# Kernel tuning notes

Measured on AMD Instinct MI355X. Metric: run time of the kernel, lower is better.

The kernel has to match this reference:

```python
import jax, jax.numpy as jnp
import numpy as np

D_IN, H1, H2, B, K = 128, 128, 64, 262144, 4

def _mk(key, shape):
    return jax.random.normal(key, shape, dtype=jnp.float32) * 0.05

def setup_inputs() -> dict:
    key = jax.random.key(0)
    ks = jax.random.split(key, 40)
    inp = {
        'x': jax.random.normal(ks[0], (B, 96), dtype=jnp.float32),
        'u': jax.random.normal(ks[1], (B, 32), dtype=jnp.float32),
        'mix_factor': jax.random.uniform(ks[2], (1,), dtype=jnp.float32),
        'teacher_P': jax.random.uniform(ks[3], (K,), dtype=jnp.float32),
    }
    # main critic params (torch Linear: W [out,in], b [out])
    dims = [(H1, D_IN), (H1, H1), (H2, H1), (1, H2)] * 2  # l1..l4, l5..l8
    for i, (o, ii) in enumerate(dims):
        inp[f'W{i+1}'] = _mk(ks[4 + 2 * i], (o, ii))
        inp[f'b{i+1}'] = _mk(ks[5 + 2 * i], (o,))
    # stacked teacher params (K teachers), only l1,l2,l3,l5,l6,l7 are used
    tdims = {'1': (H1, D_IN), '2': (H1, H1), '3': (H2, H1), '5': (H1, D_IN), '6': (H1, H1), '7': (H2, H1)}
    j = 20
    for name, (o, ii) in tdims.items():
        inp[f'tW{name}'] = _mk(ks[j], (K, o, ii)); j += 1
        inp[f'tb{name}'] = _mk(ks[j], (K, o)); j += 1
    return inp

def reference(x, u, mix_factor, teacher_P, W1, b1, W2, b2, W3, b3, W4, b4, W5, b5, W6, b6, W7, b7, W8, b8, tW1, tb1, tW2, tb2, tW3, tb3, tW5, tb5, tW6, tb6, tW7, tb7):
    m = mix_factor  # [1], broadcasts
    P = teacher_P   # [K]
    xu = jnp.concatenate([x, u], axis=1)  # [B, 128]

    lin = lambda h, W, b: h @ W.T + b
    # teacher linear on shared input [B,I] -> [K,B,O]
    tlin0 = lambda h, W, b: jnp.einsum('bi,koi->kbo', h, W) + b[:, None, :]
    # teacher linear on per-teacher streams [K,B,I] -> [K,B,O]
    tlin = lambda h, W, b: jnp.einsum('kbi,koi->kbo', h, W) + b[:, None, :]
    mixsum = lambda ht: jnp.einsum('kbo,k->bo', ht, P)

    def head(W_a, b_a, W_b, b_b, W_c, b_c, W_d, b_d, tWa, tba, tWb, tbb, tWc, tbc):
        ht = tlin0(xu, tWa, tba)                                   # [K,B,128]
        h = jax.nn.relu(lin(xu, W_a, b_a) * (1 - m) + mixsum(ht) * m)
        ht = jax.nn.relu(ht)
        ht2 = tlin(ht, tWb, tbb)
        h = jax.nn.relu(lin(h, W_b, b_b) * (1 - m) + mixsum(ht2) * m)
        ht2 = jax.nn.relu(ht2)
        ht3 = tlin(ht2, tWc, tbc)
        h = jax.nn.relu(lin(h, W_c, b_c) * (1 - m) + mixsum(ht3) * m)
        return lin(h, W_d, b_d)                                    # [B,1]

    x1 = head(W1, b1, W2, b2, W3, b3, W4, b4, tW1, tb1, tW2, tb2, tW3, tb3)
    x2 = head(W5, b5, W6, b6, W7, b7, W8, b8, tW5, tb5, tW6, tb6, tW7, tb7)
    return (x1, x2)
```

## Files before the change

kernel.cpp:

```cpp
#include <hip/hip_runtime.h>
#include <hip/hip_bf16.h>
#include <stdint.h>

#define B_TOTAL 262144
#define TB 64
#define RECORD 2560
#define LDS_BYTES 163840
#define HEAD_W 204800

typedef short v8s __attribute__((ext_vector_type(8)));
typedef float v4f __attribute__((ext_vector_type(4)));

union Frag { uint4 q; uint32_t d[4]; v8s v; };

__device__ __forceinline__ uint32_t pack2(float a, float b) {
    union { __hip_bfloat162 h; uint32_t u; } p;
    p.h = __float22bfloat162_rn(make_float2(a, b));
    return p.u;
}


struct KParams {
    const float* x; const float* u; const float* mix; const float* P;
    const float* mb[6];
    const float* tb[6];
    const float* Wout[2];
    const float* bout[2];
    const unsigned short* wbf;
    float* out;
};

struct PrepParams { const float* src[12]; unsigned short* dst; };

__global__ __launch_bounds__(256) void prep_kernel(PrepParams pp) {
    const int ends[12] = {16384,81920,98304,163840,172032,204800,
                          221184,286720,303104,368640,376832,409600};
    int gi = (blockIdx.x * 256 + threadIdx.x) * 4;
    if (gi >= 409600) return;
    int s = 0;
    #pragma unroll
    for (int i = 0; i < 12; ++i) { if (gi >= ends[i]) s = i + 1; }
    int base = (s == 0) ? 0 : ends[s - 1];
    const float4 f = *(const float4*)(pp.src[s] + (gi - base));
    *(uint2*)(pp.dst + gi) = make_uint2(pack2(f.x, f.y), pack2(f.z, f.w));
}

__device__ __forceinline__ void stage_xu(char* lds, const float* x, const float* u,
                                         int rowBase, int tid)
{
    for (int G = tid; G < 1024; G += 512) {
        const int row = G >> 4;
        const int gg  = G & 15;
        const int grow = rowBase + row;
        float4 fa, fb;
        if (gg < 12) {
            const float* s2 = x + grow * 96 + gg * 8;
            fa = *(const float4*)s2; fb = *(const float4*)(s2 + 4);
        } else {
            const float* s2 = u + grow * 32 + (gg - 12) * 8;
            fa = *(const float4*)s2; fb = *(const float4*)(s2 + 4);
        }
        *(uint4*)(lds + row * RECORD + ((gg ^ (row & 15)) << 4)) =
            make_uint4(pack2(fa.x, fa.y), pack2(fa.z, fa.w),
                       pack2(fb.x, fb.y), pack2(fb.z, fb.w));
    }
}

struct WPre { Frag w[20]; float4 mB; float4 tB[4]; };

template<int N>
__device__ __forceinline__ WPre preload(const unsigned short* W, int colBase,
        const float* mbias, const float* tbias, int lane)
{
    WPre r;
    const int l15  = lane & 15;
    const int quad = lane >> 4;
    const unsigned short* wRow = W + (colBase + l15) * 128 + quad * 8;
    #pragma unroll
    for (int s = 0; s < 5; ++s)
        #pragma unroll
        for (int ks = 0; ks < 4; ++ks)
            r.w[s * 4 + ks].q = *(const uint4*)(wRow + s * (N * 128) + ks * 32);
    const int obase = colBase + quad * 4;
    r.mB = *(const float4*)(mbias + obase);
    #pragma unroll
    for (int s = 0; s < 4; ++s)
        r.tB[s] = *(const float4*)(tbias + s * N + obase);
    return r;
}

template<bool SHARED_IN, int SM, int ST, int NBT>
__device__ __forceinline__ void mfma_phase(const char* lds, uint32_t btOff,
        const WPre& wp, v4f (&acc)[5][NBT], int lane)
{
    const int l15  = lane & 15;
    const int quad = lane >> 4;
    const uint32_t rb = (uint32_t)l15 * RECORD + ((uint32_t)l15 << 4) + btOff;
    uint32_t rA[4];
    #pragma unroll
    for (int ks = 0; ks < 4; ++ks)
        rA[ks] = rb ^ (uint32_t)(((ks << 2) | quad) << 4);

    #pragma unroll
    for (int bt = 0; bt < NBT; ++bt) {
        acc[0][bt] = (v4f){wp.mB.x, wp.mB.y, wp.mB.z, wp.mB.w};
        #pragma unroll
        for (int s = 0; s < 4; ++s)
            acc[s + 1][bt] = (v4f){wp.tB[s].x, wp.tB[s].y, wp.tB[s].z, wp.tB[s].w};
    }

    #pragma unroll
    for (int ks = 0; ks < 4; ++ks) {
        Frag xS[NBT];
        if constexpr (SHARED_IN) {
            #pragma unroll
            for (int bt = 0; bt < NBT; ++bt)
                xS[bt].q = *(const uint4*)(lds + rA[ks]
                            + (uint32_t)(bt * 40960 + SM * 256));
        }
        #pragma unroll
        for (int s = 0; s < 5; ++s) {
            constexpr int dummy = 0; (void)dummy;
            Frag xF[NBT];
            if constexpr (!SHARED_IN) {
                const int slot = (s == 0) ? SM : (ST + s - 1);
                #pragma unroll
                for (int bt = 0; bt < NBT; ++bt)
                    xF[bt].q = *(const uint4*)(lds + rA[ks]
                                + (uint32_t)(bt * 40960 + slot * 256));
            }
            #pragma unroll
            for (int bt = 0; bt < NBT; ++bt)
                acc[s][bt] = __builtin_amdgcn_mfma_f32_16x16x32_bf16(
                    wp.w[s * 4 + ks].v, (SHARED_IN ? xS[bt].v : xF[bt].v),
                    acc[s][bt], 0, 0, 0);
        }
    }
}

template<int WM, int WT>
__device__ __forceinline__ void write_streams(char* lds, v4f (&acc)[5][4],
        float c0, const float* cP, int lane, int colBase)
{
    const int l15  = lane & 15;
    const int quad = lane >> 4;
    const uint32_t rb = (uint32_t)l15 * RECORD + ((uint32_t)l15 << 4);
    const int ocg = (colBase >> 3) + (quad >> 1);
    const uint32_t w0 = (rb ^ ((uint32_t)ocg << 4)) + (uint32_t)((quad & 1) << 3);
    #pragma unroll
    for (int bt = 0; bt < 4; ++bt) {
        char* ab = lds + (w0 + (uint32_t)(bt * 40960));
        float vr[4];
        vr[0] = c0 * acc[0][bt][0];
        vr[1] = c0 * acc[0][bt][1];
        vr[2] = c0 * acc[0][bt][2];
        vr[3] = c0 * acc[0][bt][3];
        uint2 tw[4];
        #pragma unroll
        for (int s = 0; s < 4; ++s) {
            const float t0 = acc[s + 1][bt][0];
            const float t1 = acc[s + 1][bt][1];
            const float t2 = acc[s + 1][bt][2];
            const float t3 = acc[s + 1][bt][3];
            vr[0] = fmaf(cP[s], t0, vr[0]);
            vr[1] = fmaf(cP[s], t1, vr[1]);
            vr[2] = fmaf(cP[s], t2, vr[2]);
            vr[3] = fmaf(cP[s], t3, vr[3]);
            tw[s] = make_uint2(pack2(fmaxf(t0, 0.f), fmaxf(t1, 0.f)),
                               pack2(fmaxf(t2, 0.f), fmaxf(t3, 0.f)));
        }
        *(uint2*)(ab + WM * 256) =
            make_uint2(pack2(fmaxf(vr[0], 0.f), fmaxf(vr[1], 0.f)),
                       pack2(fmaxf(vr[2], 0.f), fmaxf(vr[3], 0.f)));
        #pragma unroll
        for (int s = 0; s < 4; ++s)
            *(uint2*)(ab + (WT + s) * 256) = tw[s];
    }
}

__device__ __forceinline__ void psum_write(const v4f (&accF)[5][2], float c0,
        const float* cP, const float* Wout, float* pgrid, int lane,
        int cb64, int btB64)
{
    const int obase = cb64 + ((lane >> 4) << 2);
    const float4 wo = *(const float4*)(Wout + obase);
    #pragma unroll
    for (int j = 0; j < 2; ++j) {
        float vr[4];
        vr[0] = c0 * accF[0][j][0];
        vr[1] = c0 * accF[0][j][1];
        vr[2] = c0 * accF[0][j][2];
        vr[3] = c0 * accF[0][j][3];
        #pragma unroll
        for (int s = 0; s < 4; ++s) {
            vr[0] = fmaf(cP[s], accF[s + 1][j][0], vr[0]);
            vr[1] = fmaf(cP[s], accF[s + 1][j][1], vr[1]);
            vr[2] = fmaf(cP[s], accF[s + 1][j][2], vr[2]);
            vr[3] = fmaf(cP[s], accF[s + 1][j][3], vr[3]);
        }
        float pp = fmaxf(vr[0], 0.f) * wo.x + fmaxf(vr[1], 0.f) * wo.y
                 + fmaxf(vr[2], 0.f) * wo.z + fmaxf(vr[3], 0.f) * wo.w;
        pp += __shfl_xor(pp, 16);
        pp += __shfl_xor(pp, 32);
        if (lane < 16)
            pgrid[(cb64 >> 4) * 64 + (btB64 + j) * 16 + lane] = pp;
    }
}

extern "C" __global__ __launch_bounds__(512, 2)
void critic_kernel(KParams p)
{
    extern __shared__ char lds[];
    const int tid  = threadIdx.x;
    const int lane = tid & 63;
    const int wave = tid >> 6;
    const int rowBase = blockIdx.x * TB;

    const int cb128 = wave << 4;
    const int cb64  = (wave >> 1) << 4;
    const int btB64 = (wave & 1) << 1;
    const uint32_t btOff64 = (uint32_t)btB64 * 40960u;

    const float m  = p.mix[0];
    const float c0 = 1.f - m;
    float cP[4];
    #pragma unroll
    for (int k = 0; k < 4; ++k) cP[k] = m * p.P[k];

    const unsigned short* wb0 = p.wbf;
    const unsigned short* wb1 = p.wbf + HEAD_W;

    stage_xu(lds, p.x, p.u, rowBase, tid);
    WPre wA = preload<128>(wb0, cb128, p.mb[0], p.tb[0], lane);
    __syncthreads();

    v4f accB[5][4];
    {
        WPre wB = preload<128>(wb1, cb128, p.mb[3], p.tb[3], lane);
        v4f accA[5][4];
        mfma_phase<true, 0, 0, 4>(lds, 0, wA, accA, lane);
        write_streams<1, 2>(lds, accA, c0, cP, lane, cb128);
        mfma_phase<true, 0, 0, 4>(lds, 0, wB, accB, lane);
    }
    __syncthreads();

    v4f accC[5][4];
    {
        WPre wC = preload<128>(wb0 + 81920, cb128, p.mb[1], p.tb[1], lane);
        write_streams<0, 6>(lds, accB, c0, cP, lane, cb128);
        mfma_phase<false, 1, 2, 4>(lds, 0, wC, accC, lane);
    }
    __syncthreads();

    v4f accD[5][4];
    {
        WPre wD = preload<128>(wb1 + 81920, cb128, p.mb[4], p.tb[4], lane);
        write_streams<1, 2>(lds, accC, c0, cP, lane, cb128);
        mfma_phase<false, 0, 6, 4>(lds, 0, wD, accD, lane);
    }
    __syncthreads();

    v4f accE[5][2];
    {
        WPre wE = preload<64>(wb0 + 163840, cb64, p.mb[2], p.tb[2], lane);
        write_streams<0, 6>(lds, accD, c0, cP, lane, cb128);
        mfma_phase<false, 1, 2, 2>(lds, btOff64, wE, accE, lane);
    }
    __syncthreads();

    v4f accF[5][2];
    {
        WPre wF = preload<64>(wb1 + 163840, cb64, p.mb[5], p.tb[5], lane);
        psum_write(accE, c0, cP, p.Wout[0], (float*)(lds + 256),
                   lane, cb64, btB64);
        mfma_phase<false, 0, 6, 2>(lds, btOff64, wF, accF, lane);
    }
    __syncthreads();

    if (tid < 64) {
        const float* pg = (const float*)(lds + 256);
        p.out[rowBase + tid] =
            p.bout[0][0] + pg[tid] + pg[64 + tid] + pg[128 + tid] + pg[192 + tid];
    }
    psum_write(accF, c0, cP, p.Wout[1], (float*)(lds + 1536),
               lane, cb64, btB64);
    __syncthreads();

    if (tid < 64) {
        const float* pg = (const float*)(lds + 1536);
        p.out[B_TOTAL + rowBase + tid] =
            p.bout[1][0] + pg[tid] + pg[64 + tid] + pg[128 + tid] + pg[192 + tid];
    }
}

extern "C" void kernel_launch(void* const* d_in, const int* in_sizes, int n_in,
                              void* d_out, int out_size, void* d_ws, size_t ws_size,
                              hipStream_t stream)
{
    (void)in_sizes; (void)n_in; (void)out_size; (void)ws_size;

    PrepParams pp;
    const int sidx[12] = {4, 20, 6, 22, 8, 24, 12, 26, 14, 28, 16, 30};
    for (int i = 0; i < 12; ++i) pp.src[i] = (const float*)d_in[sidx[i]];
    pp.dst = (unsigned short*)d_ws;

    KParams kp;
    kp.x = (const float*)d_in[0];  kp.u = (const float*)d_in[1];
    kp.mix = (const float*)d_in[2]; kp.P = (const float*)d_in[3];
    const int mbi[6] = {5, 7, 9, 13, 15, 17};
    const int tbi[6] = {21, 23, 25, 27, 29, 31};
    for (int i = 0; i < 6; ++i) {
        kp.mb[i] = (const float*)d_in[mbi[i]];
        kp.tb[i] = (const float*)d_in[tbi[i]];
    }
    kp.Wout[0] = (const float*)d_in[10]; kp.Wout[1] = (const float*)d_in[18];
    kp.bout[0] = (const float*)d_in[11]; kp.bout[1] = (const float*)d_in[19];
    kp.wbf = (const unsigned short*)d_ws;
    kp.out = (float*)d_out;

    (void)hipFuncSetAttribute((const void*)critic_kernel,
                              hipFuncAttributeMaxDynamicSharedMemorySize, LDS_BYTES);

    hipLaunchKernelGGL(prep_kernel, dim3(400), dim3(256), 0, stream, pp);
    hipLaunchKernelGGL(critic_kernel, dim3(B_TOTAL / TB), dim3(512), LDS_BYTES, stream, kp);
}
```

Before: 786.5 us.

## Split weight preloads across K-halves and defer bias add to epilogue

Weight fragment preloads for the next layer are split into two K-halves and interleaved with the current layer's MFMA halves, so global loads overlap matrix work across phase boundaries. Bias is no longer used to initialise the accumulators: they start at zero and bias is added in the write_streams/psum_write epilogues, which frees the bias registers during the MFMA loops. This is meant to hide global load latency and lower register pressure, but it keeps two weight sets partially live at once, which can raise VGPR usage under the 512x2 launch bounds.

```diff
diff --git a/kernel.cpp b/kernel.cpp
--- a/kernel.cpp
+++ b/kernel.cpp
@@ -66,67 +66,57 @@
     }
 }
 
-struct WPre { Frag w[20]; float4 mB; float4 tB[4]; };
-
-template<int N>
-__device__ __forceinline__ WPre preload(const unsigned short* W, int colBase,
-        const float* mbias, const float* tbias, int lane)
-{
-    WPre r;
+struct WPre { Frag w[20]; };
+
+template<int N, int KB, int KE>
+__device__ __forceinline__ void preload_ks(WPre& r, const unsigned short* W,
+        int colBase, int lane)
+{
     const int l15  = lane & 15;
     const int quad = lane >> 4;
     const unsigned short* wRow = W + (colBase + l15) * 128 + quad * 8;
     #pragma unroll
     for (int s = 0; s < 5; ++s)
         #pragma unroll
-        for (int ks = 0; ks < 4; ++ks)
+        for (int ks = KB; ks < KE; ++ks)
             r.w[s * 4 + ks].q = *(const uint4*)(wRow + s * (N * 128) + ks * 32);
-    const int obase = colBase + quad * 4;
-    r.mB = *(const float4*)(mbias + obase);
-    #pragma unroll
-    for (int s = 0; s < 4; ++s)
-        r.tB[s] = *(const float4*)(tbias + s * N + obase);
-    return r;
-}
-
-template<bool SHARED_IN, int SM, int ST, int NBT>
-__device__ __forceinline__ void mfma_phase(const char* lds, uint32_t btOff,
+}
+
+template<int NBT>
+__device__ __forceinline__ void zero_acc(v4f (&acc)[5][NBT]) {
+    #pragma unroll
+    for (int s = 0; s < 5; ++s)
+        #pragma unroll
+        for (int bt = 0; bt < NBT; ++bt)
+            acc[s][bt] = (v4f){0.f, 0.f, 0.f, 0.f};
+}
+
+template<bool SHARED_IN, int SM, int ST, int NBT, int KB, int KE>
+__device__ __forceinline__ void mfma_part(const char* lds, uint32_t btOff,
         const WPre& wp, v4f (&acc)[5][NBT], int lane)
 {
     const int l15  = lane & 15;
     const int quad = lane >> 4;
     const uint32_t rb = (uint32_t)l15 * RECORD + ((uint32_t)l15 << 4) + btOff;
-    uint32_t rA[4];
-    #pragma unroll
-    for (int ks = 0; ks < 4; ++ks)
-        rA[ks] = rb ^ (uint32_t)(((ks << 2) | quad) << 4);
-
-    #pragma unroll
-    for (int bt = 0; bt < NBT; ++bt) {
-        acc[0][bt] = (v4f){wp.mB.x, wp.mB.y, wp.mB.z, wp.mB.w};
-        #pragma unroll
-        for (int s = 0; s < 4; ++s)
-            acc[s + 1][bt] = (v4f){wp.tB[s].x, wp.tB[s].y, wp.tB[s].z, wp.tB[s].w};
-    }
-
-    #pragma unroll
-    for (int ks = 0; ks < 4; ++ks) {
+
+    #pragma unroll
+    for (int ks = KB; ks < KE; ++ks) {
+        const uint32_t rA = rb ^ (uint32_t)(((ks << 2) | quad) << 4);
         Frag xS[NBT];
         if constexpr (SHARED_IN) {
             #pragma unroll
             for (int bt = 0; bt < NBT; ++bt)
-                xS[bt].q = *(const uint4*)(lds + rA[ks]
+                xS[bt].q = *(const uint4*)(lds + rA
                             + (uint32_t)(bt * 40960 + SM * 256));
         }
         #pragma unroll
         for (int s = 0; s < 5; ++s) {
-            constexpr int dummy = 0; (void)dummy;
             Frag xF[NBT];
             if constexpr (!SHARED_IN) {
                 const int slot = (s == 0) ? SM : (ST + s - 1);
                 #pragma unroll
                 for (int bt = 0; bt < NBT; ++bt)
-                    xF[bt].q = *(const uint4*)(lds + rA[ks]
+                    xF[bt].q = *(const uint4*)(lds + rA
                                 + (uint32_t)(bt * 40960 + slot * 256));
             }
             #pragma unroll
@@ -138,12 +128,20 @@
     }
 }
 
-template<int WM, int WT>
+template<int WM, int WT, int N>
 __device__ __forceinline__ void write_streams(char* lds, v4f (&acc)[5][4],
-        float c0, const float* cP, int lane, int colBase)
+        float c0, const float* cP, int lane, int colBase,
+        const float* mbias, const float* tbias)
 {
     const int l15  = lane & 15;
     const int quad = lane >> 4;
+    const int obase = colBase + (quad << 2);
+    const float4 mB = *(const float4*)(mbias + obase);
+    float4 tB[4];
+    #pragma unroll
+    for (int s = 0; s < 4; ++s)
+        tB[s] = *(const float4*)(tbias + s * N + obase);
+
     const uint32_t rb = (uint32_t)l15 * RECORD + ((uint32_t)l15 << 4);
     const int ocg = (colBase >> 3) + (quad >> 1);
     const uint32_t w0 = (rb ^ ((uint32_t)ocg << 4)) + (uint32_t)((quad & 1) << 3);
@@ -151,17 +149,17 @@
     for (int bt = 0; bt < 4; ++bt) {
         char* ab = lds + (w0 + (uint32_t)(bt * 40960));
         float vr[4];
-        vr[0] = c0 * acc[0][bt][0];
-        vr[1] = c0 * acc[0][bt][1];
-        vr[2] = c0 * acc[0][bt][2];
-        vr[3] = c0 * acc[0][bt][3];
+        vr[0] = c0 * (acc[0][bt][0] + mB.x);
+        vr[1] = c0 * (acc[0][bt][1] + mB.y);
+        vr[2] = c0 * (acc[0][bt][2] + mB.z);
+        vr[3] = c0 * (acc[0][bt][3] + mB.w);
         uint2 tw[4];
         #pragma unroll
         for (int s = 0; s < 4; ++s) {
-            const float t0 = acc[s + 1][bt][0];
-            const float t1 = acc[s + 1][bt][1];
-            const float t2 = acc[s + 1][bt][2];
-            const float t3 = acc[s + 1][bt][3];
+            const float t0 = acc[s + 1][bt][0] + tB[s].x;
+            const float t1 = acc[s + 1][bt][1] + tB[s].y;
+            const float t2 = acc[s + 1][bt][2] + tB[s].z;
+            const float t3 = acc[s + 1][bt][3] + tB[s].w;
             vr[0] = fmaf(cP[s], t0, vr[0]);
             vr[1] = fmaf(cP[s], t1, vr[1]);
             vr[2] = fmaf(cP[s], t2, vr[2]);
@@ -179,24 +177,29 @@
 }
 
 __device__ __forceinline__ void psum_write(const v4f (&accF)[5][2], float c0,
-        const float* cP, const float* Wout, float* pgrid, int lane,
-        int cb64, int btB64)
+        const float* cP, const float* Wout, const float* mbias,
+        const float* tbias, float* pgrid, int lane, int cb64, int btB64)
 {
     const int obase = cb64 + ((lane >> 4) << 2);
+    const float4 mB = *(const float4*)(mbias + obase);
+    float4 tB[4];
+    #pragma unroll
+    for (int s = 0; s < 4; ++s)
+        tB[s] = *(const float4*)(tbias + s * 64 + obase);
     const float4 wo = *(const float4*)(Wout + obase);
     #pragma unroll
     for (int j = 0; j < 2; ++j) {
         float vr[4];
-        vr[0] = c0 * accF[0][j][0];
-        vr[1] = c0 * accF[0][j][1];
-        vr[2] = c0 * accF[0][j][2];
-        vr[3] = c0 * accF[0][j][3];
+        vr[0] = c0 * (accF[0][j][0] + mB.x);
+        vr[1] = c0 * (accF[0][j][1] + mB.y);
+        vr[2] = c0 * (accF[0][j][2] + mB.z);
+        vr[3] = c0 * (accF[0][j][3] + mB.w);
         #pragma unroll
         for (int s = 0; s < 4; ++s) {
-            vr[0] = fmaf(cP[s], accF[s + 1][j][0], vr[0]);
-            vr[1] = fmaf(cP[s], accF[s + 1][j][1], vr[1]);
-            vr[2] = fmaf(cP[s], accF[s + 1][j][2], vr[2]);
-            vr[3] = fmaf(cP[s], accF[s + 1][j][3], vr[3]);
+            vr[0] = fmaf(cP[s], accF[s + 1][j][0] + tB[s].x, vr[0]);
+            vr[1] = fmaf(cP[s], accF[s + 1][j][1] + tB[s].y, vr[1]);
+            vr[2] = fmaf(cP[s], accF[s + 1][j][2] + tB[s].z, vr[2]);
+            vr[3] = fmaf(cP[s], accF[s + 1][j][3] + tB[s].w, vr[3]);
         }
         float pp = fmaxf(vr[0], 0.f) * wo.x + fmaxf(vr[1], 0.f) * wo.y
                  + fmaxf(vr[2], 0.f) * wo.z + fmaxf(vr[3], 0.f) * wo.w;
@@ -230,50 +233,70 @@
     const unsigned short* wb0 = p.wbf;
     const unsigned short* wb1 = p.wbf + HEAD_W;
 
+    WPre wA, wB, wC, wD, wE, wF;
+
     stage_xu(lds, p.x, p.u, rowBase, tid);
-    WPre wA = preload<128>(wb0, cb128, p.mb[0], p.tb[0], lane);
+    preload_ks<128, 0, 4>(wA, wb0, cb128, lane);
     __syncthreads();
 
     v4f accB[5][4];
     {
-        WPre wB = preload<128>(wb1, cb128, p.mb[3], p.tb[3], lane);
+        preload_ks<128, 0, 2>(wB, wb1, cb128, lane);
         v4f accA[5][4];
-        mfma_phase<true, 0, 0, 4>(lds, 0, wA, accA, lane);
-        write_streams<1, 2>(lds, accA, c0, cP, lane, cb128);
-        mfma_phase<true, 0, 0, 4>(lds, 0, wB, accB, lane);
+        zero_acc(accA);
+        mfma_part<true, 0, 0, 4, 0, 2>(lds, 0, wA, accA, lane);
+        preload_ks<128, 2, 4>(wB, wb1, cb128, lane);
+        mfma_part<true, 0, 0, 4, 2, 4>(lds, 0, wA, accA, lane);
+        write_streams<1, 2, 128>(lds, accA, c0, cP, lane, cb128,
+                                 p.mb[0], p.tb[0]);
+        zero_acc(accB);
+        mfma_part<true, 0, 0, 4, 0, 4>(lds, 0, wB, accB, lane);
     }
     __syncthreads();
 
     v4f accC[5][4];
     {
-        WPre wC = preload<128>(wb0 + 81920, cb128, p.mb[1], p.tb[1], lane);
-        write_streams<0, 6>(lds, accB, c0, cP, lane, cb128);
-        mfma_phase<false, 1, 2, 4>(lds, 0, wC, accC, lane);
+        preload_ks<128, 0, 4>(wC, wb0 + 81920, cb128, lane);
+        preload_ks<128, 0, 2>(wD, wb1 + 81920, cb128, lane);
+        write_streams<0, 6, 128>(lds, accB, c0, cP, lane, cb128,
+                                 p.mb[3], p.tb[3]);
+        zero_acc(accC);
+        mfma_part<false, 1, 2, 4, 0, 2>(lds, 0, wC, accC, lane);
+        preload_ks<128, 2, 4>(wD, wb1 + 81920, cb128, lane);
+        mfma_part<false, 1, 2, 4, 2, 4>(lds, 0, wC, accC, lane);
     }
     __syncthreads();
 
     v4f accD[5][4];
     {
-        WPre wD = preload<128>(wb1 + 81920, cb128, p.mb[4], p.tb[4], lane);
-        write_streams<1, 2>(lds, accC, c0, cP, lane, cb128);
-        mfma_phase<false, 0, 6, 4>(lds, 0, wD, accD, lane);
+        preload_ks<64, 0, 2>(wE, wb0 + 163840, cb64, lane);
+        write_streams<1, 2, 128>(lds, accC, c0, cP, lane, cb128,
+                                 p.mb[1], p.tb[1]);
+        zero_acc(accD);
+        mfma_part<false, 0, 6, 4, 0, 2>(lds, 0, wD, accD, lane);
+        preload_ks<64, 2, 4>(wE, wb0 + 163840, cb64, lane);
+        mfma_part<false, 0, 6, 4, 2, 4>(lds, 0, wD, accD, lane);
     }
     __syncthreads();
 
     v4f accE[5][2];
     {
-        WPre wE = preload<64>(wb0 + 163840, cb64, p.mb[2], p.tb[2], lane);
-        write_streams<0, 6>(lds, accD, c0, cP, lane, cb128);
-        mfma_phase<false, 1, 2, 2>(lds, btOff64, wE, accE, lane);
+        preload_ks<64, 0, 2>(wF, wb1 + 163840, cb64, lane);
+        write_streams<0, 6, 128>(lds, accD, c0, cP, lane, cb128,
+                                 p.mb[4], p.tb[4]);
+        zero_acc(accE);
+        mfma_part<false, 1, 2, 2, 0, 2>(lds, btOff64, wE, accE, lane);
+        preload_ks<64, 2, 4>(wF, wb1 + 163840, cb64, lane);
+        mfma_part<false, 1, 2, 2, 2, 4>(lds, btOff64, wE, accE, lane);
     }
     __syncthreads();
 
     v4f accF[5][2];
     {
-        WPre wF = preload<64>(wb1 + 163840, cb64, p.mb[5], p.tb[5], lane);
-        psum_write(accE, c0, cP, p.Wout[0], (float*)(lds + 256),
-                   lane, cb64, btB64);
-        mfma_phase<false, 0, 6, 2>(lds, btOff64, wF, accF, lane);
+        zero_acc(accF);
+        psum_write(accE, c0, cP, p.Wout[0], p.mb[2], p.tb[2],
+                   (float*)(lds + 256), lane, cb64, btB64);
+        mfma_part<false, 0, 6, 2, 0, 4>(lds, btOff64, wF, accF, lane);
     }
     __syncthreads();
 
@@ -282,8 +305,8 @@
         p.out[rowBase + tid] =
             p.bout[0][0] + pg[tid] + pg[64 + tid] + pg[128 + tid] + pg[192 + tid];
     }
-    psum_write(accF, c0, cP, p.Wout[1], (float*)(lds + 1536),
-               lane, cb64, btB64);
+    psum_write(accF, c0, cP, p.Wout[1], p.mb[5], p.tb[5],
+               (float*)(lds + 1536), lane, cb64, btB64);
     __syncthreads();
 
     if (tid < 64) {
```

Result: slower. 817.1 us (+3.9%).
